# Performance work log

Hardware: AMD Instinct MI355X
Metric: run time of the kernel (lower is better)

The kernel has to match this reference:

```python
import jax, jax.numpy as jnp
import numpy as np

N = 1 << 20          # ray samples
POS_DIM = 32         # levels * feature_dim (hash_encoding is identity stub)
DENSITY_W = 64
COLOR_W = 64


def sh4_encoding(d):
    # Fourth-order (degree-4, 16-component) real spherical harmonics, vectorized.
    x, y, z = d[..., 0], d[..., 1], d[..., 2]
    xx, yy, zz = x * x, y * y, z * z
    c0 = jnp.full_like(x, 0.28209479177387814)
    comps = [
        c0,
        0.4886025119029199 * y,
        0.4886025119029199 * z,
        0.4886025119029199 * x,
        1.0925484305920792 * x * y,
        1.0925484305920792 * y * z,
        0.9461746957575601 * zz - 0.31539156525252,
        1.0925484305920792 * x * z,
        0.5462742152960396 * (xx - yy),
        0.5900435899266435 * y * (3 * xx - yy),
        2.890611442640554 * x * y * z,
        0.4570457994644658 * y * (5 * zz - 1),
        0.3731763325901154 * z * (5 * zz - 3),
        0.4570457994644658 * x * (5 * zz - 1),
        1.445305721320277 * z * (xx - yy),
        0.5900435899266435 * x * (xx - 3 * yy),
    ]
    return jnp.stack(comps, axis=-1)  # [..., 16]


def setup_inputs() -> dict:
    key = jax.random.key(0)
    ks = jax.random.split(key, 8)
    def dense_init(k, fan_in, fan_out):
        # flax default: lecun_normal kernel, zeros bias
        w = jax.random.normal(k, (fan_in, fan_out), dtype=jnp.float32) / np.sqrt(fan_in)
        b = jnp.zeros((fan_out,), dtype=jnp.float32)
        return w, b
    position = jax.random.normal(ks[0], (N, POS_DIM), dtype=jnp.float32)
    direction = jax.random.normal(ks[1], (N, 3), dtype=jnp.float32)
    W1, b1 = dense_init(ks[2], POS_DIM, DENSITY_W)
    W2, b2 = dense_init(ks[3], DENSITY_W, 16)
    W3, b3 = dense_init(ks[4], 16 + 16, COLOR_W)
    W4, b4 = dense_init(ks[5], COLOR_W, COLOR_W)
    W5, b5 = dense_init(ks[6], COLOR_W, 3)
    return {
        "position": position, "direction": direction,
        "W1": W1, "b1": b1, "W2": W2, "b2": b2,
        "W3": W3, "b3": b3, "W4": W4, "b4": b4,
        "W5": W5, "b5": b5,
    }


def reference(position, direction, W1, b1, W2, b2, W3, b3, W4, b4, W5, b5):
    # Density MLP
    h = jax.nn.relu(position @ W1 + b1)        # [N, 64]
    density = h @ W2 + b2                      # [N, 16]
    # Color MLP on concat(density_feat, SH(dir))
    enc_dir = sh4_encoding(direction)          # [N, 16]
    c = jnp.concatenate([density, enc_dir], axis=-1)  # [N, 32]
    c = jax.nn.relu(c @ W3 + b3)               # [N, 64]
    c = jax.nn.relu(c @ W4 + b4)               # [N, 64]
    c = c @ W5 + b5                            # [N, 3]
    color = jax.nn.sigmoid(c)                  # high_dynamic_range=False
    return (density, color)
```

## Files before the change

kernel.cpp:

```cpp
#include <hip/hip_runtime.h>
#include <hip/hip_bf16.h>

typedef __bf16 bf16_t;
typedef short  s4    __attribute__((ext_vector_type(4)));
typedef short  s8    __attribute__((ext_vector_type(8)));
typedef float  f32x4 __attribute__((ext_vector_type(4)));

#define TPW   16
#define WAVES 4
#define ROWS_PER_BLOCK (WAVES * TPW * 16)

__device__ __forceinline__ short bfs(float f) {
    return __builtin_bit_cast(short, (bf16_t)f);
}
__device__ __forceinline__ s4 pack4(f32x4 a) {
    s4 r; r[0]=bfs(a[0]); r[1]=bfs(a[1]); r[2]=bfs(a[2]); r[3]=bfs(a[3]); return r;
}
__device__ __forceinline__ s4 relu_pack4(f32x4 a) {
    s4 r;
    r[0]=bfs(fmaxf(a[0],0.f)); r[1]=bfs(fmaxf(a[1],0.f));
    r[2]=bfs(fmaxf(a[2],0.f)); r[3]=bfs(fmaxf(a[3],0.f));
    return r;
}
__device__ __forceinline__ s8 cat(s4 a, s4 b) {
    return __builtin_shufflevector(a, b, 0, 1, 2, 3, 4, 5, 6, 7);
}
#define MFMA32(a,b,c) __builtin_amdgcn_mfma_f32_16x16x32_bf16(a, b, c, 0, 0, 0)

__global__ __launch_bounds__(256) void nerf_fused(
    const float* __restrict__ pos, const float* __restrict__ dir,
    const float* __restrict__ W1, const float* __restrict__ b1,
    const float* __restrict__ W2, const float* __restrict__ b2,
    const float* __restrict__ W3, const float* __restrict__ b3,
    const float* __restrict__ W4, const float* __restrict__ b4,
    const float* __restrict__ W5, const float* __restrict__ b5,
    float* __restrict__ outD, float* __restrict__ outC)
{
    const int tid  = threadIdx.x;
    const int w    = tid >> 6;
    const int lane = tid & 63;
    const int q    = lane >> 4;
    const int n    = lane & 15;

    s8 wa1[4], wa2x[2], wa3[4], wa4x[4][2], wa5x[2];
    #pragma unroll
    for (int t = 0; t < 4; ++t)
        #pragma unroll
        for (int h = 0; h < 2; ++h)
            #pragma unroll
            for (int i = 0; i < 4; ++i)
                wa1[t][4*h+i] = bfs(W1[(16*h + 4*q + i) * 64 + 16*t + n]);
    #pragma unroll
    for (int j = 0; j < 2; ++j)
        #pragma unroll
        for (int h = 0; h < 2; ++h)
            #pragma unroll
            for (int i = 0; i < 4; ++i)
                wa2x[j][4*h+i] = bfs(W2[(16*(2*j+h) + 4*q + i) * 16 + n]);
    #pragma unroll
    for (int t = 0; t < 4; ++t)
        #pragma unroll
        for (int h = 0; h < 2; ++h)
            #pragma unroll
            for (int i = 0; i < 4; ++i)
                wa3[t][4*h+i] = bfs(W3[(16*h + 4*q + i) * 64 + 16*t + n]);
    #pragma unroll
    for (int t = 0; t < 4; ++t)
        #pragma unroll
        for (int j = 0; j < 2; ++j)
            #pragma unroll
            for (int h = 0; h < 2; ++h)
                #pragma unroll
                for (int i = 0; i < 4; ++i)
                    wa4x[t][j][4*h+i] = bfs(W4[(16*(2*j+h) + 4*q + i) * 64 + 16*t + n]);
    #pragma unroll
    for (int j = 0; j < 2; ++j)
        #pragma unroll
        for (int h = 0; h < 2; ++h)
            #pragma unroll
            for (int i = 0; i < 4; ++i)
                wa5x[j][4*h+i] = (n < 3) ? bfs(W5[(16*(2*j+h) + 4*q + i) * 3 + n])
                                         : (short)0;

    f32x4 bi1[4], bi3[4], bi4[4], bi2, bi5;
    #pragma unroll
    for (int t = 0; t < 4; ++t)
        #pragma unroll
        for (int r = 0; r < 4; ++r) {
            bi1[t][r] = b1[16*t + 4*q + r];
            bi3[t][r] = b3[16*t + 4*q + r];
            bi4[t][r] = b4[16*t + 4*q + r];
        }
    #pragma unroll
    for (int r = 0; r < 4; ++r) {
        bi2[r] = b2[4*q + r];
        bi5[r] = (q == 0 && r < 3) ? b5[r] : 0.f;
    }

    const int waveRow0 = blockIdx.x * ROWS_PER_BLOCK + w * (TPW * 16);

    const float* pp = pos  + (size_t)(waveRow0 + n) * 32 + 4*q;
    const float* dp = dir  + (size_t)(waveRow0 + n) * 3;
    float*       pD = outD + (size_t)(waveRow0 + n) * 16 + 4*q;
    float*       pC = outC + (size_t)(waveRow0 + n) * 3;

    f32x4 pa = *(const f32x4*)pp;
    f32x4 pb = *(const f32x4*)(pp + 16);
    float dx = dp[0];
    float dy = dp[1];
    float dz = dp[2];

    for (int t = 0; t < TPW; ++t) {
        const float* ppn = pp + ((t + 1 < TPW) ? 16 * 32 : 0);
        const float* dpn = dp + ((t + 1 < TPW) ? 16 * 3  : 0);
        f32x4 pa2 = *(const f32x4*)ppn;
        f32x4 pb2 = *(const f32x4*)(ppn + 16);
        float dx2 = dpn[0];
        float dy2 = dpn[1];
        float dz2 = dpn[2];

        s8 xb = cat(pack4(pa), pack4(pb));

        s4 hf[4];
        #pragma unroll
        for (int tt = 0; tt < 4; ++tt) {
            f32x4 h = MFMA32(wa1[tt], xb, bi1[tt]);
            hf[tt] = relu_pack4(h);
        }

        f32x4 d2 = MFMA32(wa2x[0], cat(hf[0], hf[1]), bi2);
        d2 = MFMA32(wa2x[1], cat(hf[2], hf[3]), d2);

        *(f32x4*)pD = d2;

        f32x4 shv;
        {
            const float xx = dx*dx, yy = dy*dy, zz = dz*dz;
            if (q == 0) {
                shv[0] = 0.28209479177387814f;
                shv[1] = 0.4886025119029199f * dy;
                shv[2] = 0.4886025119029199f * dz;
                shv[3] = 0.4886025119029199f * dx;
            } else if (q == 1) {
                shv[0] = 1.0925484305920792f * dx * dy;
                shv[1] = 1.0925484305920792f * dy * dz;
                shv[2] = 0.9461746957575601f * zz - 0.31539156525252f;
                shv[3] = 1.0925484305920792f * dx * dz;
            } else if (q == 2) {
                shv[0] = 0.5462742152960396f * (xx - yy);
                shv[1] = 0.5900435899266435f * dy * (3.f*xx - yy);
                shv[2] = 2.890611442640554f * dx * dy * dz;
                shv[3] = 0.4570457994644658f * dy * (5.f*zz - 1.f);
            } else {
                shv[0] = 0.3731763325901154f * dz * (5.f*zz - 3.f);
                shv[1] = 0.4570457994644658f * dx * (5.f*zz - 1.f);
                shv[2] = 1.445305721320277f  * dz * (xx - yy);
                shv[3] = 0.5900435899266435f * dx * (xx - 3.f*yy);
            }
        }
        s8 cf = cat(pack4(d2), pack4(shv));

        s4 gf[4];
        #pragma unroll
        for (int tt = 0; tt < 4; ++tt) {
            f32x4 g = MFMA32(wa3[tt], cf, bi3[tt]);
            gf[tt] = relu_pack4(g);
        }

        s8 gl = cat(gf[0], gf[1]), gh = cat(gf[2], gf[3]);
        s4 ef[4];
        #pragma unroll
        for (int tt = 0; tt < 4; ++tt) {
            f32x4 e = MFMA32(wa4x[tt][0], gl, bi4[tt]);
            e = MFMA32(wa4x[tt][1], gh, e);
            ef[tt] = relu_pack4(e);
        }

        f32x4 c5 = MFMA32(wa5x[0], cat(ef[0], ef[1]), bi5);
        c5 = MFMA32(wa5x[1], cat(ef[2], ef[3]), c5);

        f32x4 cv;
        cv[0] = 1.f / (1.f + __expf(-c5[0]));
        cv[1] = 1.f / (1.f + __expf(-c5[1]));
        cv[2] = 1.f / (1.f + __expf(-c5[2]));
        if (q == 0) {
            pC[0] = cv[0];
            pC[1] = cv[1];
            pC[2] = cv[2];
        }

        pp += 16 * 32; dp += 16 * 3; pD += 16 * 16; pC += 16 * 3;
        pa = pa2; pb = pb2; dx = dx2; dy = dy2; dz = dz2;
    }
}

extern "C" void kernel_launch(void* const* d_in, const int* in_sizes, int n_in,
                              void* d_out, int out_size, void* d_ws, size_t ws_size,
                              hipStream_t stream) {
    const float* pos = (const float*)d_in[0];
    const float* dir = (const float*)d_in[1];
    const float* W1  = (const float*)d_in[2];
    const float* b1  = (const float*)d_in[3];
    const float* W2  = (const float*)d_in[4];
    const float* b2  = (const float*)d_in[5];
    const float* W3  = (const float*)d_in[6];
    const float* b3  = (const float*)d_in[7];
    const float* W4  = (const float*)d_in[8];
    const float* b4  = (const float*)d_in[9];
    const float* W5  = (const float*)d_in[10];
    const float* b5  = (const float*)d_in[11];

    const int N = in_sizes[0] / 32;
    float* outD = (float*)d_out;
    float* outC = outD + (size_t)N * 16;

    const int grid = N / ROWS_PER_BLOCK;
    nerf_fused<<<grid, WAVES * 64, 0, stream>>>(pos, dir, W1, b1, W2, b2, W3, b3,
                                                W4, b4, W5, b5, outD, outC);
}
```

Measured before the change: 253.7 us.

## Stage W3/W4 fragments in LDS and interleave two row tiles per iteration

Moves the W3 and W4 bf16 weight fragments out of per-thread registers into shared memory, cooperatively loaded by the four waves, and reads them back each iteration. The main loop now handles two 16-row tiles at once (A/B), with independent MFMA chains interleaved and prefetch widened to two tiles. The aim is to cut VGPR pressure so more waves fit per CU, and to hide MFMA dependency latency through the extra instruction-level parallelism. The cost is added LDS reads every iteration and more live registers for the second tile.

```diff
diff --git a/kernel.cpp b/kernel.cpp
--- a/kernel.cpp
+++ b/kernel.cpp
@@ -36,13 +36,16 @@
     const float* __restrict__ W5, const float* __restrict__ b5,
     float* __restrict__ outD, float* __restrict__ outC)
 {
+    __shared__ s8 w3lds[4 * 64];
+    __shared__ s8 w4lds[8 * 64];
+
     const int tid  = threadIdx.x;
     const int w    = tid >> 6;
     const int lane = tid & 63;
     const int q    = lane >> 4;
     const int n    = lane & 15;
 
-    s8 wa1[4], wa2x[2], wa3[4], wa4x[4][2], wa5x[2];
+    s8 wa1[4], wa2x[2], wa5x[2];
     #pragma unroll
     for (int t = 0; t < 4; ++t)
         #pragma unroll
@@ -58,29 +61,34 @@
             for (int i = 0; i < 4; ++i)
                 wa2x[j][4*h+i] = bfs(W2[(16*(2*j+h) + 4*q + i) * 16 + n]);
     #pragma unroll
-    for (int t = 0; t < 4; ++t)
-        #pragma unroll
-        for (int h = 0; h < 2; ++h)
-            #pragma unroll
-            for (int i = 0; i < 4; ++i)
-                wa3[t][4*h+i] = bfs(W3[(16*h + 4*q + i) * 64 + 16*t + n]);
-    #pragma unroll
-    for (int t = 0; t < 4; ++t)
-        #pragma unroll
-        for (int j = 0; j < 2; ++j)
+    for (int j = 0; j < 2; ++j)
+        #pragma unroll
+        for (int h = 0; h < 2; ++h)
+            #pragma unroll
+            for (int i = 0; i < 4; ++i)
+                wa5x[j][4*h+i] = (n < 3) ? bfs(W5[(16*(2*j+h) + 4*q + i) * 3 + n])
+                                         : (short)0;
+
+    {
+        s8 tmp;
+        #pragma unroll
+        for (int h = 0; h < 2; ++h)
+            #pragma unroll
+            for (int i = 0; i < 4; ++i)
+                tmp[4*h+i] = bfs(W3[(16*h + 4*q + i) * 64 + 16*w + n]);
+        w3lds[w * 64 + lane] = tmp;
+        #pragma unroll
+        for (int cc = 0; cc < 2; ++cc) {
+            s8 t4;
             #pragma unroll
             for (int h = 0; h < 2; ++h)
                 #pragma unroll
                 for (int i = 0; i < 4; ++i)
-                    wa4x[t][j][4*h+i] = bfs(W4[(16*(2*j+h) + 4*q + i) * 64 + 16*t + n]);
-    #pragma unroll
-    for (int j = 0; j < 2; ++j)
-        #pragma unroll
-        for (int h = 0; h < 2; ++h)
-            #pragma unroll
-            for (int i = 0; i < 4; ++i)
-                wa5x[j][4*h+i] = (n < 3) ? bfs(W5[(16*(2*j+h) + 4*q + i) * 3 + n])
-                                         : (short)0;
+                    t4[4*h+i] = bfs(W4[(16*(2*cc+h) + 4*q + i) * 64 + 16*w + n]);
+            w4lds[(2*w + cc) * 64 + lane] = t4;
+        }
+    }
+    __syncthreads();
 
     f32x4 bi1[4], bi3[4], bi4[4], bi2, bi5;
     #pragma unroll
@@ -104,93 +112,141 @@
     float*       pD = outD + (size_t)(waveRow0 + n) * 16 + 4*q;
     float*       pC = outC + (size_t)(waveRow0 + n) * 3;
 
-    f32x4 pa = *(const f32x4*)pp;
-    f32x4 pb = *(const f32x4*)(pp + 16);
-    float dx = dp[0];
-    float dy = dp[1];
-    float dz = dp[2];
-
-    for (int t = 0; t < TPW; ++t) {
-        const float* ppn = pp + ((t + 1 < TPW) ? 16 * 32 : 0);
-        const float* dpn = dp + ((t + 1 < TPW) ? 16 * 3  : 0);
-        f32x4 pa2 = *(const f32x4*)ppn;
-        f32x4 pb2 = *(const f32x4*)(ppn + 16);
-        float dx2 = dpn[0];
-        float dy2 = dpn[1];
-        float dz2 = dpn[2];
-
-        s8 xb = cat(pack4(pa), pack4(pb));
-
-        s4 hf[4];
+    f32x4 paA = *(const f32x4*)pp;
+    f32x4 pbA = *(const f32x4*)(pp + 16);
+    f32x4 paB = *(const f32x4*)(pp + 512);
+    f32x4 pbB = *(const f32x4*)(pp + 528);
+    float dxA = dp[0], dyA = dp[1], dzA = dp[2];
+    float dxB = dp[48], dyB = dp[49], dzB = dp[50];
+
+    for (int t = 0; t < TPW; t += 2) {
+        const float* ppn = pp + ((t + 2 < TPW) ? 2 * 16 * 32 : 0);
+        const float* dpn = dp + ((t + 2 < TPW) ? 2 * 16 * 3  : 0);
+        f32x4 paA2 = *(const f32x4*)ppn;
+        f32x4 pbA2 = *(const f32x4*)(ppn + 16);
+        f32x4 paB2 = *(const f32x4*)(ppn + 512);
+        f32x4 pbB2 = *(const f32x4*)(ppn + 528);
+        float dxA2 = dpn[0],  dyA2 = dpn[1],  dzA2 = dpn[2];
+        float dxB2 = dpn[48], dyB2 = dpn[49], dzB2 = dpn[50];
+
+        s8 xbA = cat(pack4(paA), pack4(pbA));
+        s8 xbB = cat(pack4(paB), pack4(pbB));
+
+        s4 hfA[4], hfB[4];
         #pragma unroll
         for (int tt = 0; tt < 4; ++tt) {
-            f32x4 h = MFMA32(wa1[tt], xb, bi1[tt]);
-            hf[tt] = relu_pack4(h);
-        }
-
-        f32x4 d2 = MFMA32(wa2x[0], cat(hf[0], hf[1]), bi2);
-        d2 = MFMA32(wa2x[1], cat(hf[2], hf[3]), d2);
-
-        *(f32x4*)pD = d2;
-
-        f32x4 shv;
+            f32x4 hA = MFMA32(wa1[tt], xbA, bi1[tt]);
+            f32x4 hB = MFMA32(wa1[tt], xbB, bi1[tt]);
+            hfA[tt] = relu_pack4(hA);
+            hfB[tt] = relu_pack4(hB);
+        }
+
+        f32x4 d2A = MFMA32(wa2x[0], cat(hfA[0], hfA[1]), bi2);
+        f32x4 d2B = MFMA32(wa2x[0], cat(hfB[0], hfB[1]), bi2);
+        d2A = MFMA32(wa2x[1], cat(hfA[2], hfA[3]), d2A);
+        d2B = MFMA32(wa2x[1], cat(hfB[2], hfB[3]), d2B);
+
+        *(f32x4*)pD         = d2A;
+        *(f32x4*)(pD + 256) = d2B;
+
+        f32x4 shvA, shvB;
         {
-            const float xx = dx*dx, yy = dy*dy, zz = dz*dz;
+            const float xx = dxA*dxA, yy = dyA*dyA, zz = dzA*dzA;
             if (q == 0) {
-                shv[0] = 0.28209479177387814f;
-                shv[1] = 0.4886025119029199f * dy;
-                shv[2] = 0.4886025119029199f * dz;
-                shv[3] = 0.4886025119029199f * dx;
+                shvA[0] = 0.28209479177387814f;
+                shvA[1] = 0.4886025119029199f * dyA;
+                shvA[2] = 0.4886025119029199f * dzA;
+                shvA[3] = 0.4886025119029199f * dxA;
             } else if (q == 1) {
-                shv[0] = 1.0925484305920792f * dx * dy;
-                shv[1] = 1.0925484305920792f * dy * dz;
-                shv[2] = 0.9461746957575601f * zz - 0.31539156525252f;
-                shv[3] = 1.0925484305920792f * dx * dz;
+                shvA[0] = 1.0925484305920792f * dxA * dyA;
+                shvA[1] = 1.0925484305920792f * dyA * dzA;
+                shvA[2] = 0.9461746957575601f * zz - 0.31539156525252f;
+                shvA[3] = 1.0925484305920792f * dxA * dzA;
             } else if (q == 2) {
-                shv[0] = 0.5462742152960396f * (xx - yy);
-                shv[1] = 0.5900435899266435f * dy * (3.f*xx - yy);
-                shv[2] = 2.890611442640554f * dx * dy * dz;
-                shv[3] = 0.4570457994644658f * dy * (5.f*zz - 1.f);
+                shvA[0] = 0.5462742152960396f * (xx - yy);
+                shvA[1] = 0.5900435899266435f * dyA * (3.f*xx - yy);
+                shvA[2] = 2.890611442640554f * dxA * dyA * dzA;
+                shvA[3] = 0.4570457994644658f * dyA * (5.f*zz - 1.f);
             } else {
-                shv[0] = 0.3731763325901154f * dz * (5.f*zz - 3.f);
-                shv[1] = 0.4570457994644658f * dx * (5.f*zz - 1.f);
-                shv[2] = 1.445305721320277f  * dz * (xx - yy);
-                shv[3] = 0.5900435899266435f * dx * (xx - 3.f*yy);
+                shvA[0] = 0.3731763325901154f * dzA * (5.f*zz - 3.f);
+                shvA[1] = 0.4570457994644658f * dxA * (5.f*zz - 1.f);
+                shvA[2] = 1.445305721320277f  * dzA * (xx - yy);
+                shvA[3] = 0.5900435899266435f * dxA * (xx - 3.f*yy);
             }
         }
-        s8 cf = cat(pack4(d2), pack4(shv));
-
-        s4 gf[4];
+        {
+            const float xx = dxB*dxB, yy = dyB*dyB, zz = dzB*dzB;
+            if (q == 0) {
+                shvB[0] = 0.28209479177387814f;
+                shvB[1] = 0.4886025119029199f * dyB;
+                shvB[2] = 0.4886025119029199f * dzB;
+                shvB[3] = 0.4886025119029199f * dxB;
+            } else if (q == 1) {
+                shvB[0] = 1.0925484305920792f * dxB * dyB;
+                shvB[1] = 1.0925484305920792f * dyB * dzB;
+                shvB[2] = 0.9461746957575601f * zz - 0.31539156525252f;
+                shvB[3] = 1.0925484305920792f * dxB * dzB;
+            } else if (q == 2) {
+                shvB[0] = 0.5462742152960396f * (xx - yy);
+                shvB[1] = 0.5900435899266435f * dyB * (3.f*xx - yy);
+                shvB[2] = 2.890611442640554f * dxB * dyB * dzB;
+                shvB[3] = 0.4570457994644658f * dyB * (5.f*zz - 1.f);
+            } else {
+                shvB[0] = 0.3731763325901154f * dzB * (5.f*zz - 3.f);
+                shvB[1] = 0.4570457994644658f * dxB * (5.f*zz - 1.f);
+                shvB[2] = 1.445305721320277f  * dzB * (xx - yy);
+                shvB[3] = 0.5900435899266435f * dxB * (xx - 3.f*yy);
+            }
+        }
+        s8 cfA = cat(pack4(d2A), pack4(shvA));
+        s8 cfB = cat(pack4(d2B), pack4(shvB));
+
+        s4 gfA[4], gfB[4];
         #pragma unroll
         for (int tt = 0; tt < 4; ++tt) {
-            f32x4 g = MFMA32(wa3[tt], cf, bi3[tt]);
-            gf[tt] = relu_pack4(g);
-        }
-
-        s8 gl = cat(gf[0], gf[1]), gh = cat(gf[2], gf[3]);
-        s4 ef[4];
+            s8 wf = w3lds[tt * 64 + lane];
+            f32x4 gA = MFMA32(wf, cfA, bi3[tt]);
+            f32x4 gB = MFMA32(wf, cfB, bi3[tt]);
+            gfA[tt] = relu_pack4(gA);
+            gfB[tt] = relu_pack4(gB);
+        }
+
+        s8 glA = cat(gfA[0], gfA[1]), ghA = cat(gfA[2], gfA[3]);
+        s8 glB = cat(gfB[0], gfB[1]), ghB = cat(gfB[2], gfB[3]);
+        s4 efA[4], efB[4];
         #pragma unroll
         for (int tt = 0; tt < 4; ++tt) {
-            f32x4 e = MFMA32(wa4x[tt][0], gl, bi4[tt]);
-            e = MFMA32(wa4x[tt][1], gh, e);
-            ef[tt] = relu_pack4(e);
-        }
-
-        f32x4 c5 = MFMA32(wa5x[0], cat(ef[0], ef[1]), bi5);
-        c5 = MFMA32(wa5x[1], cat(ef[2], ef[3]), c5);
-
-        f32x4 cv;
-        cv[0] = 1.f / (1.f + __expf(-c5[0]));
-        cv[1] = 1.f / (1.f + __expf(-c5[1]));
-        cv[2] = 1.f / (1.f + __expf(-c5[2]));
+            s8 w0 = w4lds[(tt*2 + 0) * 64 + lane];
+            s8 w1 = w4lds[(tt*2 + 1) * 64 + lane];
+            f32x4 eA = MFMA32(w0, glA, bi4[tt]);
+            f32x4 eB = MFMA32(w0, glB, bi4[tt]);
+            eA = MFMA32(w1, ghA, eA);
+            eB = MFMA32(w1, ghB, eB);
+            efA[tt] = relu_pack4(eA);
+            efB[tt] = relu_pack4(eB);
+        }
+
+        f32x4 c5A = MFMA32(wa5x[0], cat(efA[0], efA[1]), bi5);
+        f32x4 c5B = MFMA32(wa5x[0], cat(efB[0], efB[1]), bi5);
+        c5A = MFMA32(wa5x[1], cat(efA[2], efA[3]), c5A);
+        c5B = MFMA32(wa5x[1], cat(efB[2], efB[3]), c5B);
+
+        f32x4 cvA, cvB;
+        cvA[0] = 1.f / (1.f + __expf(-c5A[0]));
+        cvA[1] = 1.f / (1.f + __expf(-c5A[1]));
+        cvA[2] = 1.f / (1.f + __expf(-c5A[2]));
+        cvB[0] = 1.f / (1.f + __expf(-c5B[0]));
+        cvB[1] = 1.f / (1.f + __expf(-c5B[1]));
+        cvB[2] = 1.f / (1.f + __expf(-c5B[2]));
         if (q == 0) {
-            pC[0] = cv[0];
-            pC[1] = cv[1];
-            pC[2] = cv[2];
-        }
-
-        pp += 16 * 32; dp += 16 * 3; pD += 16 * 16; pC += 16 * 3;
-        pa = pa2; pb = pb2; dx = dx2; dy = dy2; dz = dz2;
+            pC[0] = cvA[0]; pC[1] = cvA[1]; pC[2] = cvA[2];
+            pC[48] = cvB[0]; pC[49] = cvB[1]; pC[50] = cvB[2];
+        }
+
+        pp += 2 * 16 * 32; dp += 2 * 16 * 3; pD += 2 * 16 * 16; pC += 2 * 16 * 3;
+        paA = paA2; pbA = pbA2; paB = paB2; pbB = pbB2;
+        dxA = dxA2; dyA = dyA2; dzA = dzA2;
+        dxB = dxB2; dyB = dyB2; dzB = dzB2;
     }
 }
 
```

Measured after the change: 251.3 us. No clear change (-0.9%).

## Stage MLP weight fragments in LDS to cut registers and raise occupancy

Applied to the files above, without the earlier changes.

Each block now gathers the bf16 weight fragments and biases into shared memory once, cooperatively across its waves, instead of every wave holding all 20 fragments in registers. The inner loop reads fragments and biases from LDS at each MFMA, launch bounds request 6 blocks per SM, and rows per wave are halved so there are more blocks. The explicit software prefetch of the next position and direction tile is dropped and left to the extra occupancy. In exchange the loop issues many LDS reads per tile, and each block pays the weight gather and a barrier over fewer rows.

```diff
diff --git a/kernel.cpp b/kernel.cpp
--- a/kernel.cpp
+++ b/kernel.cpp
@@ -6,7 +6,7 @@
 typedef short  s8    __attribute__((ext_vector_type(8)));
 typedef float  f32x4 __attribute__((ext_vector_type(4)));
 
-#define TPW   16
+#define TPW   8
 #define WAVES 4
 #define ROWS_PER_BLOCK (WAVES * TPW * 16)
 
@@ -27,7 +27,52 @@
 }
 #define MFMA32(a,b,c) __builtin_amdgcn_mfma_f32_16x16x32_bf16(a, b, c, 0, 0, 0)
 
-__global__ __launch_bounds__(256) void nerf_fused(
+__device__ __forceinline__ s8 gather_frag(int f, int q, int n,
+    const float* W1, const float* W2, const float* W3,
+    const float* W4, const float* W5)
+{
+    s8 r;
+    if (f < 4) {
+        const int t = f;
+        #pragma unroll
+        for (int h = 0; h < 2; ++h)
+            #pragma unroll
+            for (int i = 0; i < 4; ++i)
+                r[4*h+i] = bfs(W1[(16*h + 4*q + i) * 64 + 16*t + n]);
+    } else if (f < 6) {
+        const int j = f - 4;
+        #pragma unroll
+        for (int h = 0; h < 2; ++h)
+            #pragma unroll
+            for (int i = 0; i < 4; ++i)
+                r[4*h+i] = bfs(W2[(16*(2*j+h) + 4*q + i) * 16 + n]);
+    } else if (f < 10) {
+        const int t = f - 6;
+        #pragma unroll
+        for (int h = 0; h < 2; ++h)
+            #pragma unroll
+            for (int i = 0; i < 4; ++i)
+                r[4*h+i] = bfs(W3[(16*h + 4*q + i) * 64 + 16*t + n]);
+    } else if (f < 18) {
+        const int tt = (f - 10) >> 1, j = (f - 10) & 1;
+        #pragma unroll
+        for (int h = 0; h < 2; ++h)
+            #pragma unroll
+            for (int i = 0; i < 4; ++i)
+                r[4*h+i] = bfs(W4[(16*(2*j+h) + 4*q + i) * 64 + 16*tt + n]);
+    } else {
+        const int j = f - 18;
+        #pragma unroll
+        for (int h = 0; h < 2; ++h)
+            #pragma unroll
+            for (int i = 0; i < 4; ++i)
+                r[4*h+i] = (n < 3) ? bfs(W5[(16*(2*j+h) + 4*q + i) * 3 + n])
+                                   : (short)0;
+    }
+    return r;
+}
+
+__global__ __launch_bounds__(256, 6) void nerf_fused(
     const float* __restrict__ pos, const float* __restrict__ dir,
     const float* __restrict__ W1, const float* __restrict__ b1,
     const float* __restrict__ W2, const float* __restrict__ b2,
@@ -36,61 +81,28 @@
     const float* __restrict__ W5, const float* __restrict__ b5,
     float* __restrict__ outD, float* __restrict__ outC)
 {
+    __shared__ s8    wlds[20 * 64];
+    __shared__ float blds[3 * 64];
+
     const int tid  = threadIdx.x;
     const int w    = tid >> 6;
     const int lane = tid & 63;
     const int q    = lane >> 4;
     const int n    = lane & 15;
 
-    s8 wa1[4], wa2x[2], wa3[4], wa4x[4][2], wa5x[2];
     #pragma unroll
-    for (int t = 0; t < 4; ++t)
-        #pragma unroll
-        for (int h = 0; h < 2; ++h)
-            #pragma unroll
-            for (int i = 0; i < 4; ++i)
-                wa1[t][4*h+i] = bfs(W1[(16*h + 4*q + i) * 64 + 16*t + n]);
-    #pragma unroll
-    for (int j = 0; j < 2; ++j)
-        #pragma unroll
-        for (int h = 0; h < 2; ++h)
-            #pragma unroll
-            for (int i = 0; i < 4; ++i)
-                wa2x[j][4*h+i] = bfs(W2[(16*(2*j+h) + 4*q + i) * 16 + n]);
-    #pragma unroll
-    for (int t = 0; t < 4; ++t)
-        #pragma unroll
-        for (int h = 0; h < 2; ++h)
-            #pragma unroll
-            for (int i = 0; i < 4; ++i)
-                wa3[t][4*h+i] = bfs(W3[(16*h + 4*q + i) * 64 + 16*t + n]);
-    #pragma unroll
-    for (int t = 0; t < 4; ++t)
-        #pragma unroll
-        for (int j = 0; j < 2; ++j)
-            #pragma unroll
-            for (int h = 0; h < 2; ++h)
-                #pragma unroll
-                for (int i = 0; i < 4; ++i)
-                    wa4x[t][j][4*h+i] = bfs(W4[(16*(2*j+h) + 4*q + i) * 64 + 16*t + n]);
-    #pragma unroll
-    for (int j = 0; j < 2; ++j)
-        #pragma unroll
-        for (int h = 0; h < 2; ++h)
-            #pragma unroll
-            for (int i = 0; i < 4; ++i)
-                wa5x[j][4*h+i] = (n < 3) ? bfs(W5[(16*(2*j+h) + 4*q + i) * 3 + n])
-                                         : (short)0;
-
-    f32x4 bi1[4], bi3[4], bi4[4], bi2, bi5;
-    #pragma unroll
-    for (int t = 0; t < 4; ++t)
-        #pragma unroll
-        for (int r = 0; r < 4; ++r) {
-            bi1[t][r] = b1[16*t + 4*q + r];
-            bi3[t][r] = b3[16*t + 4*q + r];
-            bi4[t][r] = b4[16*t + 4*q + r];
-        }
+    for (int f5 = 0; f5 < 5; ++f5) {
+        const int f = w * 5 + f5;
+        wlds[f * 64 + lane] = gather_frag(f, q, n, W1, W2, W3, W4, W5);
+    }
+    if (tid < 64) {
+        blds[tid]       = b1[tid];
+        blds[64 + tid]  = b3[tid];
+        blds[128 + tid] = b4[tid];
+    }
+    __syncthreads();
+
+    f32x4 bi2, bi5;
     #pragma unroll
     for (int r = 0; r < 4; ++r) {
         bi2[r] = b2[4*q + r];
@@ -104,32 +116,23 @@
     float*       pD = outD + (size_t)(waveRow0 + n) * 16 + 4*q;
     float*       pC = outC + (size_t)(waveRow0 + n) * 3;
 
-    f32x4 pa = *(const f32x4*)pp;
-    f32x4 pb = *(const f32x4*)(pp + 16);
-    float dx = dp[0];
-    float dy = dp[1];
-    float dz = dp[2];
-
     for (int t = 0; t < TPW; ++t) {
-        const float* ppn = pp + ((t + 1 < TPW) ? 16 * 32 : 0);
-        const float* dpn = dp + ((t + 1 < TPW) ? 16 * 3  : 0);
-        f32x4 pa2 = *(const f32x4*)ppn;
-        f32x4 pb2 = *(const f32x4*)(ppn + 16);
-        float dx2 = dpn[0];
-        float dy2 = dpn[1];
-        float dz2 = dpn[2];
+        f32x4 pa = *(const f32x4*)pp;
+        f32x4 pb = *(const f32x4*)(pp + 16);
+        float dx = dp[0], dy = dp[1], dz = dp[2];
 
         s8 xb = cat(pack4(pa), pack4(pb));
 
         s4 hf[4];
         #pragma unroll
         for (int tt = 0; tt < 4; ++tt) {
-            f32x4 h = MFMA32(wa1[tt], xb, bi1[tt]);
+            f32x4 bi = *(const f32x4*)(blds + 16*tt + 4*q);
+            f32x4 h  = MFMA32(wlds[tt * 64 + lane], xb, bi);
             hf[tt] = relu_pack4(h);
         }
 
-        f32x4 d2 = MFMA32(wa2x[0], cat(hf[0], hf[1]), bi2);
-        d2 = MFMA32(wa2x[1], cat(hf[2], hf[3]), d2);
+        f32x4 d2 = MFMA32(wlds[4 * 64 + lane], cat(hf[0], hf[1]), bi2);
+        d2 = MFMA32(wlds[5 * 64 + lane], cat(hf[2], hf[3]), d2);
 
         *(f32x4*)pD = d2;
 
@@ -163,7 +166,8 @@
         s4 gf[4];
         #pragma unroll
         for (int tt = 0; tt < 4; ++tt) {
-            f32x4 g = MFMA32(wa3[tt], cf, bi3[tt]);
+            f32x4 bi = *(const f32x4*)(blds + 64 + 16*tt + 4*q);
+            f32x4 g  = MFMA32(wlds[(6 + tt) * 64 + lane], cf, bi);
             gf[tt] = relu_pack4(g);
         }
 
@@ -171,13 +175,14 @@
         s4 ef[4];
         #pragma unroll
         for (int tt = 0; tt < 4; ++tt) {
-            f32x4 e = MFMA32(wa4x[tt][0], gl, bi4[tt]);
-            e = MFMA32(wa4x[tt][1], gh, e);
+            f32x4 bi = *(const f32x4*)(blds + 128 + 16*tt + 4*q);
+            f32x4 e  = MFMA32(wlds[(10 + 2*tt) * 64 + lane], gl, bi);
+            e = MFMA32(wlds[(11 + 2*tt) * 64 + lane], gh, e);
             ef[tt] = relu_pack4(e);
         }
 
-        f32x4 c5 = MFMA32(wa5x[0], cat(ef[0], ef[1]), bi5);
-        c5 = MFMA32(wa5x[1], cat(ef[2], ef[3]), c5);
+        f32x4 c5 = MFMA32(wlds[18 * 64 + lane], cat(ef[0], ef[1]), bi5);
+        c5 = MFMA32(wlds[19 * 64 + lane], cat(ef[2], ef[3]), c5);
 
         f32x4 cv;
         cv[0] = 1.f / (1.f + __expf(-c5[0]));
@@ -190,7 +195,6 @@
         }
 
         pp += 16 * 32; dp += 16 * 3; pD += 16 * 16; pC += 16 * 3;
-        pa = pa2; pb = pb2; dx = dx2; dy = dy2; dz = dz2;
     }
 }
 
```

Result: slower. 491.6 us (+93.8%).

## Move W3/W4 weights and biases to LDS and halve tiles per wave

Applied to the files above, without the earlier changes.

Layer-3 and layer-4 weight fragments and the b1/b3/b4 biases now live in shared memory, loaded cooperatively once per block, instead of sitting in registers in every wave. The aim is to lower VGPR pressure and raise occupancy. Tiles per wave drop from 16 to 8, so the grid doubles. The cost is an LDS read for every MFMA operand in the inner loop, plus more blocks each repeating the weight setup.

```diff
diff --git a/kernel.cpp b/kernel.cpp
--- a/kernel.cpp
+++ b/kernel.cpp
@@ -6,7 +6,7 @@
 typedef short  s8    __attribute__((ext_vector_type(8)));
 typedef float  f32x4 __attribute__((ext_vector_type(4)));
 
-#define TPW   16
+#define TPW   8
 #define WAVES 4
 #define ROWS_PER_BLOCK (WAVES * TPW * 16)
 
@@ -36,43 +36,57 @@
     const float* __restrict__ W5, const float* __restrict__ b5,
     float* __restrict__ outD, float* __restrict__ outC)
 {
+    __shared__ s8    w3lds[4 * 64];
+    __shared__ s8    w4lds[8 * 64];
+    __shared__ float blds[3 * 64];
+
     const int tid  = threadIdx.x;
     const int w    = tid >> 6;
     const int lane = tid & 63;
     const int q    = lane >> 4;
     const int n    = lane & 15;
 
-    s8 wa1[4], wa2x[2], wa3[4], wa4x[4][2], wa5x[2];
-    #pragma unroll
-    for (int t = 0; t < 4; ++t)
-        #pragma unroll
-        for (int h = 0; h < 2; ++h)
-            #pragma unroll
-            for (int i = 0; i < 4; ++i)
-                wa1[t][4*h+i] = bfs(W1[(16*h + 4*q + i) * 64 + 16*t + n]);
-    #pragma unroll
-    for (int j = 0; j < 2; ++j)
-        #pragma unroll
-        for (int h = 0; h < 2; ++h)
-            #pragma unroll
-            for (int i = 0; i < 4; ++i)
-                wa2x[j][4*h+i] = bfs(W2[(16*(2*j+h) + 4*q + i) * 16 + n]);
-    #pragma unroll
-    for (int t = 0; t < 4; ++t)
-        #pragma unroll
-        for (int h = 0; h < 2; ++h)
-            #pragma unroll
-            for (int i = 0; i < 4; ++i)
-                wa3[t][4*h+i] = bfs(W3[(16*h + 4*q + i) * 64 + 16*t + n]);
-    #pragma unroll
-    for (int t = 0; t < 4; ++t)
-        #pragma unroll
-        for (int j = 0; j < 2; ++j)
+    {
+        s8 tmp;
+        #pragma unroll
+        for (int h = 0; h < 2; ++h)
+            #pragma unroll
+            for (int i = 0; i < 4; ++i)
+                tmp[4*h+i] = bfs(W3[(16*h + 4*q + i) * 64 + 16*w + n]);
+        w3lds[w * 64 + lane] = tmp;
+        #pragma unroll
+        for (int cc = 0; cc < 2; ++cc) {
+            s8 t4;
             #pragma unroll
             for (int h = 0; h < 2; ++h)
                 #pragma unroll
                 for (int i = 0; i < 4; ++i)
-                    wa4x[t][j][4*h+i] = bfs(W4[(16*(2*j+h) + 4*q + i) * 64 + 16*t + n]);
+                    t4[4*h+i] = bfs(W4[(16*(2*cc+h) + 4*q + i) * 64 + 16*w + n]);
+            w4lds[(2*w + cc) * 64 + lane] = t4;
+        }
+    }
+    if (tid < 64) {
+        blds[tid]       = b1[tid];
+        blds[64 + tid]  = b3[tid];
+        blds[128 + tid] = b4[tid];
+    }
+    __syncthreads();
+
+    s8 wa1[4], wa2x[2], wa5x[2];
+    #pragma unroll
+    for (int t = 0; t < 4; ++t)
+        #pragma unroll
+        for (int h = 0; h < 2; ++h)
+            #pragma unroll
+            for (int i = 0; i < 4; ++i)
+                wa1[t][4*h+i] = bfs(W1[(16*h + 4*q + i) * 64 + 16*t + n]);
+    #pragma unroll
+    for (int j = 0; j < 2; ++j)
+        #pragma unroll
+        for (int h = 0; h < 2; ++h)
+            #pragma unroll
+            for (int i = 0; i < 4; ++i)
+                wa2x[j][4*h+i] = bfs(W2[(16*(2*j+h) + 4*q + i) * 16 + n]);
     #pragma unroll
     for (int j = 0; j < 2; ++j)
         #pragma unroll
@@ -82,15 +96,7 @@
                 wa5x[j][4*h+i] = (n < 3) ? bfs(W5[(16*(2*j+h) + 4*q + i) * 3 + n])
                                          : (short)0;
 
-    f32x4 bi1[4], bi3[4], bi4[4], bi2, bi5;
-    #pragma unroll
-    for (int t = 0; t < 4; ++t)
-        #pragma unroll
-        for (int r = 0; r < 4; ++r) {
-            bi1[t][r] = b1[16*t + 4*q + r];
-            bi3[t][r] = b3[16*t + 4*q + r];
-            bi4[t][r] = b4[16*t + 4*q + r];
-        }
+    f32x4 bi2, bi5;
     #pragma unroll
     for (int r = 0; r < 4; ++r) {
         bi2[r] = b2[4*q + r];
@@ -106,25 +112,22 @@
 
     f32x4 pa = *(const f32x4*)pp;
     f32x4 pb = *(const f32x4*)(pp + 16);
-    float dx = dp[0];
-    float dy = dp[1];
-    float dz = dp[2];
+    float dx = dp[0], dy = dp[1], dz = dp[2];
 
     for (int t = 0; t < TPW; ++t) {
         const float* ppn = pp + ((t + 1 < TPW) ? 16 * 32 : 0);
         const float* dpn = dp + ((t + 1 < TPW) ? 16 * 3  : 0);
         f32x4 pa2 = *(const f32x4*)ppn;
         f32x4 pb2 = *(const f32x4*)(ppn + 16);
-        float dx2 = dpn[0];
-        float dy2 = dpn[1];
-        float dz2 = dpn[2];
+        float dx2 = dpn[0], dy2 = dpn[1], dz2 = dpn[2];
 
         s8 xb = cat(pack4(pa), pack4(pb));
 
         s4 hf[4];
         #pragma unroll
         for (int tt = 0; tt < 4; ++tt) {
-            f32x4 h = MFMA32(wa1[tt], xb, bi1[tt]);
+            f32x4 bi = *(const f32x4*)(blds + 16*tt + 4*q);
+            f32x4 h  = MFMA32(wa1[tt], xb, bi);
             hf[tt] = relu_pack4(h);
         }
 
@@ -163,7 +166,8 @@
         s4 gf[4];
         #pragma unroll
         for (int tt = 0; tt < 4; ++tt) {
-            f32x4 g = MFMA32(wa3[tt], cf, bi3[tt]);
+            f32x4 bi = *(const f32x4*)(blds + 64 + 16*tt + 4*q);
+            f32x4 g  = MFMA32(w3lds[tt * 64 + lane], cf, bi);
             gf[tt] = relu_pack4(g);
         }
 
@@ -171,8 +175,9 @@
         s4 ef[4];
         #pragma unroll
         for (int tt = 0; tt < 4; ++tt) {
-            f32x4 e = MFMA32(wa4x[tt][0], gl, bi4[tt]);
-            e = MFMA32(wa4x[tt][1], gh, e);
+            f32x4 bi = *(const f32x4*)(blds + 128 + 16*tt + 4*q);
+            f32x4 e  = MFMA32(w4lds[(2*tt + 0) * 64 + lane], gl, bi);
+            e = MFMA32(w4lds[(2*tt + 1) * 64 + lane], gh, e);
             ef[tt] = relu_pack4(e);
         }
 
```

Measured after the change: 264.1 us. +4.1%, slower.
